# Kernel optimization log

Measured on AMD Instinct MI355X. Metric: run time of the kernel, lower is better.

## Reference

```python
import jax, jax.numpy as jnp
import numpy as np

B, T_ENC, T_DEC = 16, 256, 200
E, ATT, PRE, H, MEL, LOC, K = 512, 128, 256, 1024, 80, 32, 31


def setup_inputs() -> dict:
    key = jax.random.key(0)
    ks = jax.random.split(key, 20)
    s = lambda k, shape: jax.random.normal(k, shape, jnp.float32) * 0.02
    return dict(
        encoder_output=jax.random.normal(ks[0], (B, T_ENC, E), jnp.float32),
        padded_mels=jax.random.normal(ks[1], (B, T_DEC, MEL), jnp.float32),
        enc_proj_w=s(ks[2], (ATT, E)),
        lstm_proj_w=s(ks[3], (ATT, H)),
        loc_conv_w=s(ks[4], (LOC, 1, K)),
        loc_conv_b=jnp.zeros((LOC,), jnp.float32),
        loc_dense_w=s(ks[5], (ATT, LOC)),
        loc_dense_b=jnp.zeros((ATT,), jnp.float32),
        e_w=s(ks[6], (1, ATT)),
        e_b=jnp.zeros((1,), jnp.float32),
        prenet1_w=s(ks[7], (PRE, MEL)),
        prenet2_w=s(ks[8], (PRE, PRE)),
        w_ih0=s(ks[9], (4 * H, PRE + E)),
        w_hh0=s(ks[10], (4 * H, H)),
        b_ih0=jnp.zeros((4 * H,), jnp.float32),
        b_hh0=jnp.zeros((4 * H,), jnp.float32),
        w_ih1=s(ks[11], (4 * H, H)),
        w_hh1=s(ks[12], (4 * H, H)),
        b_ih1=jnp.zeros((4 * H,), jnp.float32),
        b_hh1=jnp.zeros((4 * H,), jnp.float32),
        proj_w=s(ks[13], (MEL, H + E)),
        proj_b=jnp.zeros((MEL,), jnp.float32),
        stop_w=s(ks[14], (1, H + E)),
        stop_b=jnp.zeros((1,), jnp.float32),
        text_lengths=jax.random.randint(ks[15], (B,), T_ENC // 2, T_ENC + 1),
    )


def _lstm_cell_zero(x, w_ih, b_ih, b_hh):
    # PyTorch LSTM cell with zero initial (h, c): h_prev contributes nothing
    # except the recurrent bias b_hh. Gate order: i, f, g, o.
    g = x @ w_ih.T + b_ih + b_hh
    i, f, gg, o = jnp.split(g, 4, axis=-1)
    c = jax.nn.sigmoid(i) * jnp.tanh(gg)  # f * c_prev == 0
    return jax.nn.sigmoid(o) * jnp.tanh(c)


def reference(encoder_output, padded_mels, enc_proj_w, lstm_proj_w, loc_conv_w,
              loc_conv_b, loc_dense_w, loc_dense_b, e_w, e_b, prenet1_w,
              prenet2_w, w_ih0, w_hh0, b_ih0, b_hh0, w_ih1, w_hh1, b_ih1,
              b_hh1, proj_w, proj_b, stop_w, stop_b, text_lengths):
    b, t_enc, _ = encoder_output.shape
    n_mel = padded_mels.shape[-1]
    h = w_hh0.shape[-1]
    pad = (loc_conv_w.shape[-1] - 1) // 2
    proc_enc = encoder_output @ enc_proj_w.T              # [B,Te,128]
    mask = jnp.arange(t_enc)[None, :] < text_lengths[:, None]
    # teacher forcing (ratio=1.0): prev mel at step t is padded_mels[:, t-1]
    prev_mels = jnp.concatenate(
        [jnp.zeros((b, 1, n_mel), padded_mels.dtype), padded_mels[:, :-1]],
        axis=1).transpose(1, 0, 2)                        # [Td,B,80]

    def step(carry, prev_mel):
        awc, h2 = carry                                   # [B,Te], [B,1024]
        # prenet (dropout omitted for a deterministic reference)
        x = jax.nn.relu(prev_mel @ prenet1_w.T)
        x = jax.nn.relu(x @ prenet2_w.T)                  # [B,256]
        # location-sensitive attention
        q = h2 @ lstm_proj_w.T                            # [B,128]
        loc = jax.lax.conv_general_dilated(
            awc[:, None, :], loc_conv_w, (1,), [(pad, pad)],
            dimension_numbers=('NCH', 'OIH', 'NCH')) + loc_conv_b[None, :, None]
        loc = jnp.einsum('bct,ac->bta', loc, loc_dense_w) + loc_dense_b
        en = jnp.tanh(q[:, None, :] + loc + proc_enc) @ e_w[0] + e_b[0]
        en = jnp.where(mask, en, -1e9)
        aw = jax.nn.softmax(en, axis=-1)                  # [B,Te]
        ctx = jnp.einsum('bt,bte->be', aw, encoder_output)  # [B,512]
        # 2-layer LSTM, state reset to zero every step (as in the original)
        li = jnp.concatenate([x, ctx], axis=-1)           # [B,768]
        h1 = _lstm_cell_zero(li, w_ih0, b_ih0, b_hh0)
        h2n = _lstm_cell_zero(h1, w_ih1, b_ih1, b_hh1)
        dec = jnp.concatenate([h2n, ctx], axis=-1)        # [B,1536]
        mel = dec @ proj_w.T + proj_b                     # [B,80]
        stop = (dec @ stop_w.T + stop_b)[:, 0]            # [B]
        return (awc + aw, h2n), (mel, stop)

    init = (jnp.zeros((b, t_enc), encoder_output.dtype),
            jnp.zeros((b, h), encoder_output.dtype))
    _, (mels, stops) = jax.lax.scan(step, init, prev_mels)
    return mels.transpose(1, 0, 2), stops.T               # [B,Td,80], [B,Td]
```

## Files before the change

kernel.cpp:

```cpp
#include <hip/hip_runtime.h>
#include <math.h>

#define NB   16
#define TE   256
#define TD   200
#define EE   512
#define ATT  128
#define PREN 256
#define HH   1024
#define NMEL 80
#define NLOC 32
#define KWW  31
#define PADW 15

#define OFF_X2H  0
#define OFF_PE   (OFF_X2H + TD*NB*128)
#define OFF_ENR  (OFF_PE + NB*TE*ATT)
#define OFF_CTR  (OFF_ENR + NB*16*6*4)
#define OFF_H1H  (OFF_CTR + NB*128*4)
#define OFF_H2R  (OFF_H1H + NB*512)
#define OFF_QVR  (OFF_H2R + NB*256*4)
#define OFF_BAR  (OFF_QVR + NB*16*2*4)
#define BAR_U32  4096
#define ARR_G 0

#define LW0X_U32 (12*128)
#define LW0C_U32 (12*256)
#define LW1_U32  (12*512)
#define DYN_BYTES ((LW0X_U32 + LW0C_U32 + LW1_U32)*4)

typedef float f4 __attribute__((ext_vector_type(4)));
typedef unsigned int u32x4 __attribute__((ext_vector_type(4)));
typedef unsigned int u32x2 __attribute__((ext_vector_type(2)));
typedef _Float16 h2t __attribute__((ext_vector_type(2)));

__device__ __forceinline__ float sigmf(float x) { return 1.0f / (1.0f + expf(-x)); }
__device__ __forceinline__ float dot4(f4 a, f4 b) {
  return a.x*b.x + a.y*b.y + a.z*b.z + a.w*b.w;
}
__device__ __forceinline__ float red32(float v) {
  v += __shfl_down(v, 16, 32); v += __shfl_down(v, 8, 32);
  v += __shfl_down(v, 4, 32);  v += __shfl_down(v, 2, 32);
  v += __shfl_down(v, 1, 32);
  return v;
}
__device__ __forceinline__ float red64(float v) {
  v += __shfl_down(v, 32); v += __shfl_down(v, 16); v += __shfl_down(v, 8);
  v += __shfl_down(v, 4);  v += __shfl_down(v, 2);  v += __shfl_down(v, 1);
  return v;
}
__device__ __forceinline__ float fdot2(unsigned a, unsigned b, float c) {
  return __builtin_amdgcn_fdot2(__builtin_bit_cast(h2t, a),
                                __builtin_bit_cast(h2t, b), c, false);
}
__device__ __forceinline__ unsigned pkh(float a, float b) {
  h2t h; h.x = (_Float16)a; h.y = (_Float16)b;
  return __builtin_bit_cast(unsigned, h);
}
__device__ __forceinline__ float hlo(unsigned u) {
  return (float)__builtin_bit_cast(h2t, u).x;
}
__device__ __forceinline__ float hhi(unsigned u) {
  return (float)__builtin_bit_cast(h2t, u).y;
}

__device__ __forceinline__ unsigned ld_cg_u32(const unsigned* p) {
  unsigned r;
  asm volatile("global_load_dword %0, %1, off sc0 sc1\n\ts_waitcnt vmcnt(0)"
               : "=v"(r) : "v"(p) : "memory");
  return r;
}
__device__ __forceinline__ void st_cg_u32(unsigned* p, unsigned v) {
  asm volatile("global_store_dword %0, %1, off sc0 sc1" :: "v"(p), "v"(v) : "memory");
}
__device__ __forceinline__ f4 ld_cg_f4(const f4* p) {
  f4 r;
  asm volatile("global_load_dwordx4 %0, %1, off sc0 sc1\n\ts_waitcnt vmcnt(0)"
               : "=v"(r) : "v"(p) : "memory");
  return r;
}
__device__ __forceinline__ void st_cg_f4(f4* p, f4 v) {
  asm volatile("global_store_dwordx4 %0, %1, off sc0 sc1" :: "v"(p), "v"(v) : "memory");
}
__device__ __forceinline__ u32x4 ld_cg_u4(const void* p) {
  u32x4 r;
  asm volatile("global_load_dwordx4 %0, %1, off sc0 sc1\n\ts_waitcnt vmcnt(0)"
               : "=v"(r) : "v"(p) : "memory");
  return r;
}
__device__ __forceinline__ void st_cg_u4(void* p, u32x4 v) {
  asm volatile("global_store_dwordx4 %0, %1, off sc0 sc1" :: "v"(p), "v"(v) : "memory");
}
__device__ __forceinline__ void st_cg_u2(void* p, u32x2 v) {
  asm volatile("global_store_dwordx2 %0, %1, off sc0 sc1" :: "v"(p), "v"(v) : "memory");
}
__device__ __forceinline__ void ld4u(u32x4& a, u32x4& b, u32x4& c, u32x4& d,
                                     const void* pa, const void* pb,
                                     const void* pc, const void* pd) {
  asm volatile(
    "global_load_dwordx4 %0, %4, off sc0 sc1\n\t"
    "global_load_dwordx4 %1, %5, off sc0 sc1\n\t"
    "global_load_dwordx4 %2, %6, off sc0 sc1\n\t"
    "global_load_dwordx4 %3, %7, off sc0 sc1\n\t"
    "s_waitcnt vmcnt(0)"
    : "=&v"(a), "=&v"(b), "=&v"(c), "=&v"(d)
    : "v"(pa), "v"(pb), "v"(pc), "v"(pd) : "memory");
}

__device__ __forceinline__ void g_arrive(unsigned* bar, unsigned e) {
  __syncthreads();
  if (threadIdx.x == 0) st_cg_u32(bar + ARR_G + blockIdx.x * 16, e);
}
__device__ __forceinline__ void g_wait(unsigned* bar, unsigned e) {
  if (threadIdx.x < 256) {
    while (ld_cg_u32(bar + ARR_G + threadIdx.x * 16) < e) {}
  }
  __syncthreads();
}

__global__ void k_init(float* __restrict__ ws) {
  const int gid = blockIdx.x * 256 + threadIdx.x;
  f4* enr = (f4*)(ws + OFF_ENR);
  u32x4* ctr = (u32x4*)(ws + OFF_CTR);
  f4* h2r = (f4*)(ws + OFF_H2R);
  f4* qvr = (f4*)(ws + OFF_QVR);
  unsigned* bar = (unsigned*)(ws + OFF_BAR);
  const f4 z = (f4){0.f, 0.f, 0.f, 0.f};
  const u32x4 zu = (u32x4){0u, 0u, 0u, 0u};
  for (int i = gid; i < NB*16*6; i += 32*256) st_cg_f4(enr + i, z);
  for (int i = gid; i < NB*128; i += 32*256) st_cg_u4(ctr + i, zu);
  for (int i = gid; i < NB*256; i += 32*256) st_cg_f4(h2r + i, z);
  for (int i = gid; i < NB*32; i += 32*256) st_cg_f4(qvr + i, z);
  for (int i = gid; i < BAR_U32; i += 32*256) st_cg_u32(bar + i, 0u);
}

__global__ void k_prenet(const float* __restrict__ mels,
                         const float* __restrict__ w1,
                         const float* __restrict__ w2,
                         float* __restrict__ ws) {
  const int t = blockIdx.x >> 4;
  const int b = blockIdx.x & 15;
  const int j = threadIdx.x;
  __shared__ float s_in[NMEL];
  __shared__ float s_x1[PREN];
  if (j < NMEL) s_in[j] = (t == 0) ? 0.0f : mels[(b*TD + (t-1))*NMEL + j];
  __syncthreads();
  float a1 = 0.0f;
  #pragma unroll 8
  for (int k = 0; k < NMEL; ++k) a1 += s_in[k] * w1[j*NMEL + k];
  s_x1[j] = fmaxf(a1, 0.0f);
  __syncthreads();
  float a2 = 0.0f;
  #pragma unroll 8
  for (int k = 0; k < PREN; ++k) a2 += s_x1[k] * w2[j*PREN + k];
  ((_Float16*)(ws + OFF_X2H))[((size_t)t*NB + b)*256 + j] = (_Float16)fmaxf(a2, 0.0f);
}

__global__ void k_procenc(const float* __restrict__ enc,
                          const float* __restrict__ w,
                          float* __restrict__ pe) {
  const int bt = blockIdx.x;
  const int a = threadIdx.x;
  __shared__ float s_e[EE];
  for (int k = a; k < EE; k += 128) s_e[k] = enc[bt*EE + k];
  __syncthreads();
  float acc = 0.0f;
  #pragma unroll 8
  for (int k = 0; k < EE; ++k) acc += s_e[k] * w[a*EE + k];
  pe[bt*ATT + a] = acc;
}

__global__ void __launch_bounds__(512, 1) k_main(
    const float* __restrict__ enc,
    const float* __restrict__ lstm_proj_w,
    const float* __restrict__ loc_conv_w,
    const float* __restrict__ loc_conv_b,
    const float* __restrict__ loc_dense_w,
    const float* __restrict__ loc_dense_b,
    const float* __restrict__ e_w,
    const float* __restrict__ e_b,
    const float* __restrict__ w_ih0,
    const float* __restrict__ b_ih0,
    const float* __restrict__ b_hh0,
    const float* __restrict__ w_ih1,
    const float* __restrict__ b_ih1,
    const float* __restrict__ b_hh1,
    const float* __restrict__ proj_w,
    const float* __restrict__ proj_b,
    const float* __restrict__ stop_w,
    const float* __restrict__ stop_b,
    const int*   __restrict__ text_len,
    float* __restrict__ ws,
    float* __restrict__ out) {
  const int bid = blockIdx.x;
  const int tid = threadIdx.x;

  const unsigned* x2h = (const unsigned*)(ws + OFF_X2H);
  float* pe  = ws + OFF_PE;
  f4* en_rec = (f4*)(ws + OFF_ENR);
  u32x4* ct_rec = (u32x4*)(ws + OFF_CTR);
  unsigned* h1h = (unsigned*)(ws + OFF_H1H);
  f4* h2_rec = (f4*)(ws + OFF_H2R);
  f4* qv_rec = (f4*)(ws + OFF_QVR);
  unsigned* bar = (unsigned*)(ws + OFF_BAR);

  __shared__ __align__(16) float s_ldw[NLOC*ATT];
  __shared__ float s_awcf[TE];
  __shared__ float s_loc[16*33];
  __shared__ float s_red[16];
  __shared__ float s_en[256];
  __shared__ float s_aw[256];
  __shared__ float s_entmp[16];
  __shared__ float s_qtmp[8];
  __shared__ float s_ctmp[32];
  __shared__ __align__(16) float s_q[ATT];
  __shared__ __align__(16) float s_dec[HH+EE];
  __shared__ float s_b0[12], s_b1[12];
  extern __shared__ __align__(16) unsigned dynlds_u[];
  unsigned* lw0x = dynlds_u;
  unsigned* lw0c = lw0x + LW0X_U32;
  unsigned* lw1  = lw0c + LW0C_U32;

  const int b_grp = bid & 15;
  const int sub   = bid >> 4;
  const int h0    = bid * 4;

  for (int i = tid; i < NLOC*ATT; i += 512) {
    int c = i >> 7, a = i & 127;
    s_ldw[i] = loc_dense_w[a*NLOC + c];
  }
  if (tid < 12) {
    int g = tid >> 2, h = tid & 3;
    int gr = (g == 0 ? 0 : (g == 1 ? 2048 : 3072)) + h0 + h;
    s_b0[tid] = b_ih0[gr] + b_hh0[gr];
    s_b1[tid] = b_ih1[gr] + b_hh1[gr];
  }
  for (int i = tid; i < LW0X_U32; i += 512) {
    int r = i >> 7, c = i & 127;
    int g = r >> 2, h = r & 3;
    int grow = (g == 0 ? 0 : (g == 1 ? 2048 : 3072)) + h0 + h;
    const float* wr = w_ih0 + (size_t)grow*768;
    lw0x[i] = pkh(wr[2*c], wr[2*c+1]);
  }
  for (int i = tid; i < LW0C_U32; i += 512) {
    int r = i >> 8, c = i & 255;
    int g = r >> 2, h = r & 3;
    int grow = (g == 0 ? 0 : (g == 1 ? 2048 : 3072)) + h0 + h;
    const float* wr = w_ih0 + (size_t)grow*768 + 256;
    lw0c[i] = pkh(wr[2*c], wr[2*c+1]);
  }
  for (int i = tid; i < LW1_U32; i += 512) {
    int r = i >> 9, c = i & 511;
    int g = r >> 2, h = r & 3;
    int grow = (g == 0 ? 0 : (g == 1 ? 2048 : 3072)) + h0 + h;
    const float* wr = w_ih1 + (size_t)grow*1024;
    lw1[i] = pkh(wr[2*c], wr[2*c+1]);
  }
  if (tid < 256) s_awcf[tid] = 0.0f;

  const int   lenb = text_len[b_grp];
  const float eb0  = e_b[0];
  const int tl = tid >> 5;
  const int j  = tid & 31;
  float lcw_r[KWW];
  #pragma unroll
  for (int k = 0; k < KWW; ++k) lcw_r[k] = loc_conv_w[j*KWW + k];
  const float lcb_r = loc_conv_b[j];
  const f4 db_r = *(const f4*)(loc_dense_b + 4*j);
  const f4 ew_r = *(const f4*)(e_w + 4*j);
  const f4 pe_r = *(const f4*)(pe + (size_t)(b_grp*TE + sub*16 + tl)*ATT + 4*j);
  const f4 ps_r = pe_r + db_r;
  const int e4i = tid >> 6;
  const int ts  = tid & 63;
  f4 encr[4];
  {
    const f4* enc4 = (const f4*)(enc + (size_t)b_grp*TE*EE);
    #pragma unroll
    for (int i = 0; i < 4; ++i)
      encr[i] = enc4[(size_t)(ts + 64*i)*(EE/4) + sub*8 + e4i];
  }
  const int en_si = tid / 6;
  const int en_rr = tid - en_si*6;
  const f4* en_myrec = en_rec + (b_grp*16 + en_si)*6 + en_rr;
  const int pb = tid >> 5;
  const int kc = tid & 31;
  const u32x4* ct_my = ct_rec + pb*128;
  __syncthreads();

  unsigned eg = 0;

  for (int t = 0; t < TD; ++t) {
    const unsigned tg = (unsigned)(t + 1);
    f4 pre;
    {
      float cv = lcb_r;
      const int pos = sub*16 + tl;
      #pragma unroll
      for (int k = 0; k < KWW; ++k) {
        const int g = pos - PADW + k;
        const float av = (g >= 0 && g < TE) ? s_awcf[g] : 0.0f;
        cv += av * lcw_r[k];
      }
      s_loc[tl*33 + j] = cv;
      __syncthreads();
      f4 d4 = (f4){0.f, 0.f, 0.f, 0.f};
      #pragma unroll 8
      for (int c = 0; c < NLOC; ++c) {
        const float lv = s_loc[tl*33 + c];
        const f4 w4 = ((const f4*)s_ldw)[c*32 + j];
        d4.x += lv*w4.x; d4.y += lv*w4.y; d4.z += lv*w4.z; d4.w += lv*w4.w;
      }
      pre = ps_r + d4;
    }
    {
      if (tid < 32) {
        const int src = tid >> 1, r = tid & 1;
        const f4* qp = qv_rec + (b_grp*16 + src)*2 + r;
        f4 v;
        do { v = ld_cg_f4(qp); } while (__float_as_uint(v.z) != (unsigned)t);
        const unsigned u0 = __float_as_uint(v.x), u1 = __float_as_uint(v.y);
        const int base = src*8 + r*4;
        s_q[base+0] = hlo(u0); s_q[base+1] = hhi(u0);
        s_q[base+2] = hlo(u1); s_q[base+3] = hhi(u1);
      }
      __syncthreads();
      const f4 q4 = *(const f4*)(s_q + 4*j);
      float acc = tanhf(pre.x+q4.x)*ew_r.x + tanhf(pre.y+q4.y)*ew_r.y
                + tanhf(pre.z+q4.z)*ew_r.z + tanhf(pre.w+q4.w)*ew_r.w;
      acc = red32(acc);
      if (j == 0) {
        float evv = acc + eb0;
        const int tt = sub*16 + tl;
        if (tt >= lenb) evv = -1e9f;
        s_entmp[tl] = evv;
      }
      __syncthreads();
      if (tid < 6) {
        f4 r = (f4){0.f, 0.f, 0.f, __uint_as_float(tg)};
        const int base = 3*tid;
        r.x = s_entmp[base];
        if (base + 1 < 16) r.y = s_entmp[base+1];
        if (base + 2 < 16) r.z = s_entmp[base+2];
        st_cg_f4(en_rec + (b_grp*16 + sub)*6 + tid, r);
      }
    }
    {
      if (tid < 96) {
        f4 v;
        do { v = ld_cg_f4(en_myrec); } while (__float_as_uint(v.w) != tg);
        const int base = en_si*16 + 3*en_rr;
        s_en[base] = v.x;
        if (3*en_rr + 1 < 16) s_en[base+1] = v.y;
        if (3*en_rr + 2 < 16) s_en[base+2] = v.z;
      } else if (t > 0 && tid >= 128 && tid < 320) {
        const int ol = (tid - 128) >> 5, kq = tid & 31;
        const int m = sub*6 + ol;
        if (m < 81) {
          const float* wrow = (m < NMEL) ? (proj_w + (size_t)m*(HH+EE)) : stop_w;
          const f4* w4 = (const f4*)wrow;
          const f4* s4 = (const f4*)s_dec;
          float a2 = 0.0f;
          #pragma unroll
          for (int i = 0; i < 12; ++i) a2 += dot4(s4[kq + 32*i], w4[kq + 32*i]);
          a2 = red32(a2);
          if (kq == 0) {
            if (m < NMEL) out[(b_grp*TD + (t-1))*NMEL + m] = a2 + proj_b[m];
            else          out[NB*TD*NMEL + b_grp*TD + (t-1)] = a2 + stop_b[0];
          }
        }
      }
      __syncthreads();
      float evv = 0.f, p = 0.f;
      if (tid < 256) {
        evv = s_en[tid];
        float m = evv;
        #pragma unroll
        for (int d = 32; d > 0; d >>= 1) m = fmaxf(m, __shfl_xor(m, d));
        if ((tid & 63) == 0) s_red[tid >> 6] = m;
      }
      __syncthreads();
      const float mx = fmaxf(fmaxf(s_red[0], s_red[1]), fmaxf(s_red[2], s_red[3]));
      if (tid < 256) {
        p = expf(evv - mx);
        float sm = p;
        #pragma unroll
        for (int d = 32; d > 0; d >>= 1) sm += __shfl_xor(sm, d);
        if ((tid & 63) == 0) s_red[8 + (tid >> 6)] = sm;
      }
      __syncthreads();
      const float inv = 1.0f / (s_red[8] + s_red[9] + s_red[10] + s_red[11]);
      if (tid < 256) {
        const float aw = p * inv;
        s_aw[tid] = aw;
        s_awcf[tid] += aw;
      }
      __syncthreads();
      f4 a4 = (f4){0.f, 0.f, 0.f, 0.f};
      #pragma unroll
      for (int i = 0; i < 4; ++i) {
        const float awv = s_aw[ts + 64*i];
        a4.x += awv*encr[i].x; a4.y += awv*encr[i].y;
        a4.z += awv*encr[i].z; a4.w += awv*encr[i].w;
      }
      a4.x = red64(a4.x); a4.y = red64(a4.y); a4.z = red64(a4.z); a4.w = red64(a4.w);
      if (ts == 0) {
        s_ctmp[e4i*4+0] = a4.x; s_ctmp[e4i*4+1] = a4.y;
        s_ctmp[e4i*4+2] = a4.z; s_ctmp[e4i*4+3] = a4.w;
      }
      __syncthreads();
      if (tid < 8) {
        u32x4 w;
        w.x = pkh(s_ctmp[4*tid+0], s_ctmp[4*tid+1]);
        w.y = pkh(s_ctmp[4*tid+2], s_ctmp[4*tid+3]);
        w.z = tg; w.w = 0u;
        st_cg_u4(ct_rec + b_grp*128 + sub*8 + tid, w);
      }
    }
    float acc[12];
    {
      #pragma unroll
      for (int r = 0; r < 12; ++r) acc[r] = 0.0f;
      const u32x4 xv = ((const u32x4*)x2h)[((size_t)t*NB + pb)*32 + kc];
      #pragma unroll
      for (int r = 0; r < 12; ++r) {
        const u32x4 w = ((const u32x4*)lw0x)[r*32 + kc];
        acc[r] = fdot2(xv.x, w.x, acc[r]); acc[r] = fdot2(xv.y, w.y, acc[r]);
        acc[r] = fdot2(xv.z, w.z, acc[r]); acc[r] = fdot2(xv.w, w.w, acc[r]);
      }
    }
    {
      u32x4 ra, rb, rc, rd;
      for (;;) {
        ld4u(ra, rb, rc, rd, ct_my + 2*kc, ct_my + 2*kc + 1,
             ct_my + 2*kc + 64, ct_my + 2*kc + 65);
        if (ra.z == tg && rb.z == tg && rc.z == tg && rd.z == tg) break;
        __builtin_amdgcn_s_sleep(1);
      }
      const u32x4 c0 = (u32x4){ra.x, ra.y, rb.x, rb.y};
      const u32x4 c1 = (u32x4){rc.x, rc.y, rd.x, rd.y};
      #pragma unroll
      for (int r = 0; r < 12; ++r) {
        const u32x4 w0 = ((const u32x4*)lw0c)[r*64 + kc];
        const u32x4 w1 = ((const u32x4*)lw0c)[r*64 + kc + 32];
        acc[r] = fdot2(c0.x, w0.x, acc[r]); acc[r] = fdot2(c0.y, w0.y, acc[r]);
        acc[r] = fdot2(c0.z, w0.z, acc[r]); acc[r] = fdot2(c0.w, w0.w, acc[r]);
        acc[r] = fdot2(c1.x, w1.x, acc[r]); acc[r] = fdot2(c1.y, w1.y, acc[r]);
        acc[r] = fdot2(c1.z, w1.z, acc[r]); acc[r] = fdot2(c1.w, w1.w, acc[r]);
      }
      #pragma unroll
      for (int r = 0; r < 12; ++r) acc[r] = red32(acc[r]);
      if (kc == 0) {
        float hv[4];
        #pragma unroll
        for (int h = 0; h < 4; ++h) {
          const float gi = acc[h]   + s_b0[h];
          const float gg = acc[4+h] + s_b0[4+h];
          const float go = acc[8+h] + s_b0[8+h];
          hv[h] = sigmf(go) * tanhf(sigmf(gi) * tanhf(gg));
        }
        u32x2 stv; stv.x = pkh(hv[0], hv[1]); stv.y = pkh(hv[2], hv[3]);
        st_cg_u2((u32x2*)h1h + pb*256 + bid, stv);
      }
    }
    g_arrive(bar, ++eg);
    g_wait(bar, eg);
    {
      #pragma unroll
      for (int r = 0; r < 12; ++r) acc[r] = 0.0f;
      u32x4 v0, v1, v2, v3;
      const u32x4* hp = (const u32x4*)h1h + pb*128 + kc;
      ld4u(v0, v1, v2, v3, hp, hp+32, hp+64, hp+96);
      #pragma unroll
      for (int r = 0; r < 12; ++r) {
        const u32x4* wp = (const u32x4*)lw1 + r*128 + kc;
        const u32x4 w0 = wp[0], w1 = wp[32], w2 = wp[64], w3 = wp[96];
        acc[r] = fdot2(v0.x, w0.x, acc[r]); acc[r] = fdot2(v0.y, w0.y, acc[r]);
        acc[r] = fdot2(v0.z, w0.z, acc[r]); acc[r] = fdot2(v0.w, w0.w, acc[r]);
        acc[r] = fdot2(v1.x, w1.x, acc[r]); acc[r] = fdot2(v1.y, w1.y, acc[r]);
        acc[r] = fdot2(v1.z, w1.z, acc[r]); acc[r] = fdot2(v1.w, w1.w, acc[r]);
        acc[r] = fdot2(v2.x, w2.x, acc[r]); acc[r] = fdot2(v2.y, w2.y, acc[r]);
        acc[r] = fdot2(v2.z, w2.z, acc[r]); acc[r] = fdot2(v2.w, w2.w, acc[r]);
        acc[r] = fdot2(v3.x, w3.x, acc[r]); acc[r] = fdot2(v3.y, w3.y, acc[r]);
        acc[r] = fdot2(v3.z, w3.z, acc[r]); acc[r] = fdot2(v3.w, w3.w, acc[r]);
      }
      #pragma unroll
      for (int r = 0; r < 12; ++r) acc[r] = red32(acc[r]);
      if (kc == 0) {
        float hv[4];
        #pragma unroll
        for (int h = 0; h < 4; ++h) {
          const float gi = acc[h]   + s_b1[h];
          const float gg = acc[4+h] + s_b1[4+h];
          const float go = acc[8+h] + s_b1[8+h];
          hv[h] = sigmf(go) * tanhf(sigmf(gi) * tanhf(gg));
        }
        f4 r;
        r.x = __uint_as_float(pkh(hv[0], hv[1]));
        r.y = __uint_as_float(pkh(hv[2], hv[3]));
        r.z = __uint_as_float(tg); r.w = 0.f;
        st_cg_f4(h2_rec + pb*256 + bid, r);
      }
    }
    {
      if (tid < 256) {
        const f4* hp = h2_rec + b_grp*256 + tid;
        f4 v;
        do { v = ld_cg_f4(hp); } while (__float_as_uint(v.z) != tg);
        const unsigned u0 = __float_as_uint(v.x), u1 = __float_as_uint(v.y);
        s_dec[4*tid+0] = hlo(u0); s_dec[4*tid+1] = hhi(u0);
        s_dec[4*tid+2] = hlo(u1); s_dec[4*tid+3] = hhi(u1);
      } else if (tid < 384) {
        const int i = tid - 256;
        const u32x4* cp = ct_rec + b_grp*128 + i;
        u32x4 v;
        do { v = ld_cg_u4(cp); } while (v.z != tg);
        s_dec[HH + 4*i + 0] = hlo(v.x); s_dec[HH + 4*i + 1] = hhi(v.x);
        s_dec[HH + 4*i + 2] = hlo(v.y); s_dec[HH + 4*i + 3] = hhi(v.y);
      }
      __syncthreads();
      const int row = tid >> 6;
      const int kq  = tid & 63;
      const int a   = sub*8 + row;
      const f4* w4 = (const f4*)(lstm_proj_w + (size_t)a*HH);
      const f4* s4 = (const f4*)s_dec;
      float a2 = 0.0f;
      #pragma unroll
      for (int i = 0; i < 4; ++i) a2 += dot4(s4[kq + 64*i], w4[kq + 64*i]);
      a2 = red64(a2);
      if (kq == 0) s_qtmp[row] = a2;
      __syncthreads();
      if (tid < 2) {
        f4 r;
        r.x = __uint_as_float(pkh(s_qtmp[4*tid+0], s_qtmp[4*tid+1]));
        r.y = __uint_as_float(pkh(s_qtmp[4*tid+2], s_qtmp[4*tid+3]));
        r.z = __uint_as_float(tg); r.w = 0.f;
        st_cg_f4(qv_rec + (b_grp*16 + sub)*2 + tid, r);
      }
    }
  }
  __syncthreads();
  {
    const int ol = tid >> 5, kq = tid & 31;
    if (ol < 6) {
      const int m = sub*6 + ol;
      if (m < 81) {
        const float* wrow = (m < NMEL) ? (proj_w + (size_t)m*(HH+EE)) : stop_w;
        const f4* w4 = (const f4*)wrow;
        const f4* s4 = (const f4*)s_dec;
        float a2 = 0.0f;
        #pragma unroll
        for (int i = 0; i < 12; ++i) a2 += dot4(s4[kq + 32*i], w4[kq + 32*i]);
        a2 = red32(a2);
        if (kq == 0) {
          if (m < NMEL) out[(b_grp*TD + (TD-1))*NMEL + m] = a2 + proj_b[m];
          else          out[NB*TD*NMEL + b_grp*TD + (TD-1)] = a2 + stop_b[0];
        }
      }
    }
  }
}

extern "C" void kernel_launch(void* const* d_in, const int* in_sizes, int n_in,
                              void* d_out, int out_size, void* d_ws, size_t ws_size,
                              hipStream_t stream) {
  (void)in_sizes; (void)n_in; (void)out_size; (void)ws_size;
  const float* enc         = (const float*)d_in[0];
  const float* mels        = (const float*)d_in[1];
  const float* enc_proj_w  = (const float*)d_in[2];
  const float* lstm_proj_w = (const float*)d_in[3];
  const float* loc_conv_w  = (const float*)d_in[4];
  const float* loc_conv_b  = (const float*)d_in[5];
  const float* loc_dense_w = (const float*)d_in[6];
  const float* loc_dense_b = (const float*)d_in[7];
  const float* e_w         = (const float*)d_in[8];
  const float* e_b         = (const float*)d_in[9];
  const float* prenet1_w   = (const float*)d_in[10];
  const float* prenet2_w   = (const float*)d_in[11];
  const float* w_ih0       = (const float*)d_in[12];
  const float* b_ih0       = (const float*)d_in[14];
  const float* b_hh0       = (const float*)d_in[15];
  const float* w_ih1       = (const float*)d_in[16];
  const float* b_ih1       = (const float*)d_in[18];
  const float* b_hh1       = (const float*)d_in[19];
  const float* proj_w      = (const float*)d_in[20];
  const float* proj_b      = (const float*)d_in[21];
  const float* stop_w      = (const float*)d_in[22];
  const float* stop_b      = (const float*)d_in[23];
  const int*   text_len    = (const int*)d_in[24];
  float* ws  = (float*)d_ws;
  float* out = (float*)d_out;

  static int attr_set = 0;
  if (!attr_set) {
    hipFuncSetAttribute((const void*)k_main,
                        hipFuncAttributeMaxDynamicSharedMemorySize, DYN_BYTES);
    attr_set = 1;
  }

  k_init<<<dim3(32), dim3(256), 0, stream>>>(ws);
  k_prenet<<<dim3(TD*NB), dim3(256), 0, stream>>>(mels, prenet1_w, prenet2_w, ws);
  k_procenc<<<dim3(NB*TE), dim3(128), 0, stream>>>(enc, enc_proj_w, ws + OFF_PE);

  k_main<<<dim3(256), dim3(512), DYN_BYTES, stream>>>(
      enc, lstm_proj_w, loc_conv_w, loc_conv_b, loc_dense_w, loc_dense_b,
      e_w, e_b, w_ih0, b_ih0, b_hh0, w_ih1, b_ih1, b_hh1,
      proj_w, proj_b, stop_w, stop_b, text_len, ws, out);
}
```

Measured before the change: 3.991 ms.

## Replace grid barrier before LSTM layer 1 with per-record timestamp flags

Removes the global arrive/wait barrier between the first and second LSTM layers. Each block now writes its layer-0 hidden values together with the step tag in a 16-byte record, and consumers spin only on the specific records they need until the tags match. This cuts the all-to-all barrier latency in favour of fine-grained dataflow synchronisation, at the cost of doubled record storage, polling traffic, and reliance on 16-byte stores being observed atomically.

```diff
diff --git a/kernel.cpp b/kernel.cpp
--- a/kernel.cpp
+++ b/kernel.cpp
@@ -17,12 +17,9 @@
 #define OFF_PE   (OFF_X2H + TD*NB*128)
 #define OFF_ENR  (OFF_PE + NB*TE*ATT)
 #define OFF_CTR  (OFF_ENR + NB*16*6*4)
-#define OFF_H1H  (OFF_CTR + NB*128*4)
-#define OFF_H2R  (OFF_H1H + NB*512)
+#define OFF_H1R  (OFF_CTR + NB*128*4)
+#define OFF_H2R  (OFF_H1R + NB*256*4)
 #define OFF_QVR  (OFF_H2R + NB*256*4)
-#define OFF_BAR  (OFF_QVR + NB*16*2*4)
-#define BAR_U32  4096
-#define ARR_G 0
 
 #define LW0X_U32 (12*128)
 #define LW0C_U32 (12*256)
@@ -31,7 +28,6 @@
 
 typedef float f4 __attribute__((ext_vector_type(4)));
 typedef unsigned int u32x4 __attribute__((ext_vector_type(4)));
-typedef unsigned int u32x2 __attribute__((ext_vector_type(2)));
 typedef _Float16 h2t __attribute__((ext_vector_type(2)));
 
 __device__ __forceinline__ float sigmf(float x) { return 1.0f / (1.0f + expf(-x)); }
@@ -90,9 +86,6 @@
 }
 __device__ __forceinline__ void st_cg_u4(void* p, u32x4 v) {
   asm volatile("global_store_dwordx4 %0, %1, off sc0 sc1" :: "v"(p), "v"(v) : "memory");
-}
-__device__ __forceinline__ void st_cg_u2(void* p, u32x2 v) {
-  asm volatile("global_store_dwordx2 %0, %1, off sc0 sc1" :: "v"(p), "v"(v) : "memory");
 }
 __device__ __forceinline__ void ld4u(u32x4& a, u32x4& b, u32x4& c, u32x4& d,
                                      const void* pa, const void* pb,
@@ -107,31 +100,20 @@
     : "v"(pa), "v"(pb), "v"(pc), "v"(pd) : "memory");
 }
 
-__device__ __forceinline__ void g_arrive(unsigned* bar, unsigned e) {
-  __syncthreads();
-  if (threadIdx.x == 0) st_cg_u32(bar + ARR_G + blockIdx.x * 16, e);
-}
-__device__ __forceinline__ void g_wait(unsigned* bar, unsigned e) {
-  if (threadIdx.x < 256) {
-    while (ld_cg_u32(bar + ARR_G + threadIdx.x * 16) < e) {}
-  }
-  __syncthreads();
-}
-
 __global__ void k_init(float* __restrict__ ws) {
   const int gid = blockIdx.x * 256 + threadIdx.x;
   f4* enr = (f4*)(ws + OFF_ENR);
   u32x4* ctr = (u32x4*)(ws + OFF_CTR);
+  u32x4* h1r = (u32x4*)(ws + OFF_H1R);
   f4* h2r = (f4*)(ws + OFF_H2R);
   f4* qvr = (f4*)(ws + OFF_QVR);
-  unsigned* bar = (unsigned*)(ws + OFF_BAR);
   const f4 z = (f4){0.f, 0.f, 0.f, 0.f};
   const u32x4 zu = (u32x4){0u, 0u, 0u, 0u};
   for (int i = gid; i < NB*16*6; i += 32*256) st_cg_f4(enr + i, z);
   for (int i = gid; i < NB*128; i += 32*256) st_cg_u4(ctr + i, zu);
+  for (int i = gid; i < NB*256; i += 32*256) st_cg_u4(h1r + i, zu);
   for (int i = gid; i < NB*256; i += 32*256) st_cg_f4(h2r + i, z);
   for (int i = gid; i < NB*32; i += 32*256) st_cg_f4(qvr + i, z);
-  for (int i = gid; i < BAR_U32; i += 32*256) st_cg_u32(bar + i, 0u);
 }
 
 __global__ void k_prenet(const float* __restrict__ mels,
@@ -199,10 +181,9 @@
   float* pe  = ws + OFF_PE;
   f4* en_rec = (f4*)(ws + OFF_ENR);
   u32x4* ct_rec = (u32x4*)(ws + OFF_CTR);
-  unsigned* h1h = (unsigned*)(ws + OFF_H1H);
+  u32x4* h1_rec = (u32x4*)(ws + OFF_H1R);
   f4* h2_rec = (f4*)(ws + OFF_H2R);
   f4* qv_rec = (f4*)(ws + OFF_QVR);
-  unsigned* bar = (unsigned*)(ws + OFF_BAR);
 
   __shared__ __align__(16) float s_ldw[NLOC*ATT];
   __shared__ float s_awcf[TE];
@@ -285,9 +266,8 @@
   const int pb = tid >> 5;
   const int kc = tid & 31;
   const u32x4* ct_my = ct_rec + pb*128;
+  const u32x4* h1_my = h1_rec + pb*256;
   __syncthreads();
-
-  unsigned eg = 0;
 
   for (int t = 0; t < TD; ++t) {
     const unsigned tg = (unsigned)(t + 1);
@@ -458,18 +438,33 @@
           const float go = acc[8+h] + s_b0[8+h];
           hv[h] = sigmf(go) * tanhf(sigmf(gi) * tanhf(gg));
         }
-        u32x2 stv; stv.x = pkh(hv[0], hv[1]); stv.y = pkh(hv[2], hv[3]);
-        st_cg_u2((u32x2*)h1h + pb*256 + bid, stv);
-      }
-    }
-    g_arrive(bar, ++eg);
-    g_wait(bar, eg);
+        u32x4 r;
+        r.x = pkh(hv[0], hv[1]); r.y = pkh(hv[2], hv[3]);
+        r.z = tg; r.w = 0u;
+        st_cg_u4(h1_rec + pb*256 + bid, r);
+      }
+    }
     {
       #pragma unroll
       for (int r = 0; r < 12; ++r) acc[r] = 0.0f;
-      u32x4 v0, v1, v2, v3;
-      const u32x4* hp = (const u32x4*)h1h + pb*128 + kc;
-      ld4u(v0, v1, v2, v3, hp, hp+32, hp+64, hp+96);
+      u32x4 ra, rb, rc, rd;
+      for (;;) {
+        ld4u(ra, rb, rc, rd, h1_my + 2*kc, h1_my + 2*kc + 1,
+             h1_my + 2*kc + 64, h1_my + 2*kc + 65);
+        if (ra.z == tg && rb.z == tg && rc.z == tg && rd.z == tg) break;
+        __builtin_amdgcn_s_sleep(1);
+      }
+      const u32x4 v0 = (u32x4){ra.x, ra.y, rb.x, rb.y};
+      const u32x4 v1 = (u32x4){rc.x, rc.y, rd.x, rd.y};
+      u32x4 re, rf, rg, rh;
+      for (;;) {
+        ld4u(re, rf, rg, rh, h1_my + 2*kc + 128, h1_my + 2*kc + 129,
+             h1_my + 2*kc + 192, h1_my + 2*kc + 193);
+        if (re.z == tg && rf.z == tg && rg.z == tg && rh.z == tg) break;
+        __builtin_amdgcn_s_sleep(1);
+      }
+      const u32x4 v2 = (u32x4){re.x, re.y, rf.x, rf.y};
+      const u32x4 v3 = (u32x4){rg.x, rg.y, rh.x, rh.y};
       #pragma unroll
       for (int r = 0; r < 12; ++r) {
         const u32x4* wp = (const u32x4*)lw1 + r*128 + kc;
```

Result: slower. 5.412 ms (+35.6%).

## Use fast exp/tanh, drop softmax max pass, add L2-scoped record polling

Applied to the files above, without the earlier changes.

Replaces expf/tanhf with __expf-based fast sigmoid and tanh in the attention energy and LSTM gates. Removes the max-subtraction pass and one barrier from the softmax, relying on energies being small. Adds double stores (an L2-scoped store plus a system-coherent store) and first-poll L2-scoped loads for the inter-block records, to cut cross-block handoff latency in the persistent step loop. This risks overflow if energies grow large, and the weaker-scope first reads may be stale and fall back to the coherent loads.

```diff
diff --git a/kernel.cpp b/kernel.cpp
--- a/kernel.cpp
+++ b/kernel.cpp
@@ -34,7 +34,8 @@
 typedef unsigned int u32x2 __attribute__((ext_vector_type(2)));
 typedef _Float16 h2t __attribute__((ext_vector_type(2)));
 
-__device__ __forceinline__ float sigmf(float x) { return 1.0f / (1.0f + expf(-x)); }
+__device__ __forceinline__ float fast_sigm(float x) { return 1.0f / (1.0f + __expf(-x)); }
+__device__ __forceinline__ float fast_tanh(float x) { return 1.0f - 2.0f / (__expf(2.0f*x) + 1.0f); }
 __device__ __forceinline__ float dot4(f4 a, f4 b) {
   return a.x*b.x + a.y*b.y + a.z*b.z + a.w*b.w;
 }
@@ -93,6 +94,24 @@
 }
 __device__ __forceinline__ void st_cg_u2(void* p, u32x2 v) {
   asm volatile("global_store_dwordx2 %0, %1, off sc0 sc1" :: "v"(p), "v"(v) : "memory");
+}
+__device__ __forceinline__ f4 ld_l2_f4(const f4* p) {
+  f4 r;
+  asm volatile("global_load_dwordx4 %0, %1, off sc0\n\ts_waitcnt vmcnt(0)"
+               : "=v"(r) : "v"(p) : "memory");
+  return r;
+}
+__device__ __forceinline__ void st_l2_f4(f4* p, f4 v) {
+  asm volatile("global_store_dwordx4 %0, %1, off sc0" :: "v"(p), "v"(v) : "memory");
+}
+__device__ __forceinline__ u32x4 ld_l2_u4(const void* p) {
+  u32x4 r;
+  asm volatile("global_load_dwordx4 %0, %1, off sc0\n\ts_waitcnt vmcnt(0)"
+               : "=v"(r) : "v"(p) : "memory");
+  return r;
+}
+__device__ __forceinline__ void st_l2_u4(void* p, u32x4 v) {
+  asm volatile("global_store_dwordx4 %0, %1, off sc0" :: "v"(p), "v"(v) : "memory");
 }
 __device__ __forceinline__ void ld4u(u32x4& a, u32x4& b, u32x4& c, u32x4& d,
                                      const void* pa, const void* pb,
@@ -316,8 +335,8 @@
       if (tid < 32) {
         const int src = tid >> 1, r = tid & 1;
         const f4* qp = qv_rec + (b_grp*16 + src)*2 + r;
-        f4 v;
-        do { v = ld_cg_f4(qp); } while (__float_as_uint(v.z) != (unsigned)t);
+        f4 v = ld_l2_f4(qp);
+        while (__float_as_uint(v.z) != (unsigned)t) v = ld_cg_f4(qp);
         const unsigned u0 = __float_as_uint(v.x), u1 = __float_as_uint(v.y);
         const int base = src*8 + r*4;
         s_q[base+0] = hlo(u0); s_q[base+1] = hhi(u0);
@@ -325,8 +344,8 @@
       }
       __syncthreads();
       const f4 q4 = *(const f4*)(s_q + 4*j);
-      float acc = tanhf(pre.x+q4.x)*ew_r.x + tanhf(pre.y+q4.y)*ew_r.y
-                + tanhf(pre.z+q4.z)*ew_r.z + tanhf(pre.w+q4.w)*ew_r.w;
+      float acc = fast_tanh(pre.x+q4.x)*ew_r.x + fast_tanh(pre.y+q4.y)*ew_r.y
+                + fast_tanh(pre.z+q4.z)*ew_r.z + fast_tanh(pre.w+q4.w)*ew_r.w;
       acc = red32(acc);
       if (j == 0) {
         float evv = acc + eb0;
@@ -341,13 +360,15 @@
         r.x = s_entmp[base];
         if (base + 1 < 16) r.y = s_entmp[base+1];
         if (base + 2 < 16) r.z = s_entmp[base+2];
-        st_cg_f4(en_rec + (b_grp*16 + sub)*6 + tid, r);
+        f4* dst = en_rec + (b_grp*16 + sub)*6 + tid;
+        st_l2_f4(dst, r);
+        st_cg_f4(dst, r);
       }
     }
     {
       if (tid < 96) {
-        f4 v;
-        do { v = ld_cg_f4(en_myrec); } while (__float_as_uint(v.w) != tg);
+        f4 v = ld_l2_f4(en_myrec);
+        while (__float_as_uint(v.w) != tg) v = ld_cg_f4(en_myrec);
         const int base = en_si*16 + 3*en_rr;
         s_en[base] = v.x;
         if (3*en_rr + 1 < 16) s_en[base+1] = v.y;
@@ -370,18 +391,9 @@
         }
       }
       __syncthreads();
-      float evv = 0.f, p = 0.f;
+      float p = 0.f;
       if (tid < 256) {
-        evv = s_en[tid];
-        float m = evv;
-        #pragma unroll
-        for (int d = 32; d > 0; d >>= 1) m = fmaxf(m, __shfl_xor(m, d));
-        if ((tid & 63) == 0) s_red[tid >> 6] = m;
-      }
-      __syncthreads();
-      const float mx = fmaxf(fmaxf(s_red[0], s_red[1]), fmaxf(s_red[2], s_red[3]));
-      if (tid < 256) {
-        p = expf(evv - mx);
+        p = __expf(s_en[tid]);
         float sm = p;
         #pragma unroll
         for (int d = 32; d > 0; d >>= 1) sm += __shfl_xor(sm, d);
@@ -413,7 +425,9 @@
         w.x = pkh(s_ctmp[4*tid+0], s_ctmp[4*tid+1]);
         w.y = pkh(s_ctmp[4*tid+2], s_ctmp[4*tid+3]);
         w.z = tg; w.w = 0u;
-        st_cg_u4(ct_rec + b_grp*128 + sub*8 + tid, w);
+        u32x4* dst = ct_rec + b_grp*128 + sub*8 + tid;
+        st_l2_u4(dst, w);
+        st_cg_u4(dst, w);
       }
     }
     float acc[12];
@@ -456,7 +470,7 @@
           const float gi = acc[h]   + s_b0[h];
           const float gg = acc[4+h] + s_b0[4+h];
           const float go = acc[8+h] + s_b0[8+h];
-          hv[h] = sigmf(go) * tanhf(sigmf(gi) * tanhf(gg));
+          hv[h] = fast_sigm(go) * fast_tanh(fast_sigm(gi) * fast_tanh(gg));
         }
         u32x2 stv; stv.x = pkh(hv[0], hv[1]); stv.y = pkh(hv[2], hv[3]);
         st_cg_u2((u32x2*)h1h + pb*256 + bid, stv);
@@ -492,7 +506,7 @@
           const float gi = acc[h]   + s_b1[h];
           const float gg = acc[4+h] + s_b1[4+h];
           const float go = acc[8+h] + s_b1[8+h];
-          hv[h] = sigmf(go) * tanhf(sigmf(gi) * tanhf(gg));
+          hv[h] = fast_sigm(go) * fast_tanh(fast_sigm(gi) * fast_tanh(gg));
         }
         f4 r;
         r.x = __uint_as_float(pkh(hv[0], hv[1]));
@@ -512,8 +526,8 @@
       } else if (tid < 384) {
         const int i = tid - 256;
         const u32x4* cp = ct_rec + b_grp*128 + i;
-        u32x4 v;
-        do { v = ld_cg_u4(cp); } while (v.z != tg);
+        u32x4 v = ld_l2_u4(cp);
+        while (v.z != tg) v = ld_cg_u4(cp);
         s_dec[HH + 4*i + 0] = hlo(v.x); s_dec[HH + 4*i + 1] = hhi(v.x);
         s_dec[HH + 4*i + 2] = hlo(v.y); s_dec[HH + 4*i + 3] = hhi(v.y);
       }
@@ -534,7 +548,9 @@
         r.x = __uint_as_float(pkh(s_qtmp[4*tid+0], s_qtmp[4*tid+1]));
         r.y = __uint_as_float(pkh(s_qtmp[4*tid+2], s_qtmp[4*tid+3]));
         r.z = __uint_as_float(tg); r.w = 0.f;
-        st_cg_f4(qv_rec + (b_grp*16 + sub)*2 + tid, r);
+        f4* dst = qv_rec + (b_grp*16 + sub)*2 + tid;
+        st_l2_f4(dst, r);
+        st_cg_f4(dst, r);
       }
     }
   }
```

Result: faster. 3.719 ms (-6.8%).
